# Optimization experiments

Measured on AMD Instinct MI355X. Metric: run time of the kernel, lower is better.

Reference implementation:

```python
import jax, jax.numpy as jnp
import numpy as np

B, H, N, C = 32768, 1024, 4, 1000
BN_EPS = 1e-5        # weighted batch norm epsilon
IG_EPS = 1e-30       # info-gain log epsilon (as in CIGN repo)
TEMPERATURE = 1.0    # routing temperature
BALANCE = 2.0        # information gain balance coefficient


def setup_inputs() -> dict:
    key = jax.random.key(0)
    k = jax.random.split(key, 4)
    return {
        "ig_mask": jax.random.randint(k[0], (B,), 0, 2, dtype=jnp.int32),
        "h_net": jax.random.normal(k[1], (B, H), dtype=jnp.float32),
        "labels": jax.random.randint(k[2], (B,), 0, C, dtype=jnp.int32),
        "gamma": jnp.ones((H,), jnp.float32),
        "beta": jnp.zeros((H,), jnp.float32),
        "W": jax.random.normal(k[3], (H, N), dtype=jnp.float32) * 0.03,
        "b": jnp.zeros((N,), jnp.float32),
    }


def _weighted_batch_norm(x, mask_f, gamma, beta):
    # mask-weighted batch statistics; normalization applied to ALL samples
    w = mask_f[:, None]                       # [B,1]
    wsum = jnp.sum(mask_f)
    mean = jnp.sum(w * x, axis=0) / wsum      # [H]
    var = jnp.sum(w * (x - mean) ** 2, axis=0) / wsum
    return gamma * (x - mean) * jax.lax.rsqrt(var + BN_EPS) + beta


def _info_gain(activations, labels, mask_f):
    sample_count = jnp.sum(mask_f)
    pv = mask_f / sample_count                              # [B]
    p_n_given_x = jax.nn.softmax(activations / TEMPERATURE, axis=1)  # [B,N]
    onehot = jax.nn.one_hot(labels, C, dtype=activations.dtype)      # [B,C]
    # joint p(c,n) = sum_b pv[b] * onehot[b,c] * p_n_given_x[b,n]
    p_cn = jnp.einsum('b,bc,bn->cn', pv, onehot, p_n_given_x)        # [C,N]
    p_n = jnp.sum(p_cn, axis=0)                                      # [N]
    p_c = jnp.sum(p_cn, axis=1)                                      # [C]
    kv = p_cn * (jnp.log(p_cn + IG_EPS)
                 - jnp.log(p_c + IG_EPS)[:, None]
                 - BALANCE * jnp.log(p_n + IG_EPS)[None, :])
    return -jnp.sum(kv)


def reference(ig_mask, h_net, labels, gamma, beta, W, b):
    mask_f = ig_mask.astype(jnp.float32)
    h_normed = _weighted_batch_norm(h_net, mask_f, gamma, beta)      # [B,H]
    activations = h_normed @ W + b                                   # [B,N]
    ig_value = _info_gain(activations, labels, mask_f)               # scalar
    routing = jax.nn.one_hot(jnp.argmax(activations, axis=1), N, dtype=jnp.int32)
    out_routing = jnp.logical_and(routing.astype(bool),
                                  ig_mask[:, None].astype(bool)).astype(jnp.int32)
    return h_normed, ig_value, out_routing
```

## Files before the change

### kernel.cpp

```cpp
#include <hip/hip_runtime.h>
#include <cstddef>

#define B_SZ 32768
#define H_SZ 1024
#define N_SZ 4
#define C_SZ 1000
#define ROW_BLOCKS 2048
#define ROWS_PER_BLOCK 16

#define PART_SUM   0
#define PART_SQ    (PART_SUM + ROW_BLOCKS*H_SZ)
#define WSUM_PART  (PART_SQ  + ROW_BLOCKS*H_SZ)
#define A_OFF      (WSUM_PART + ROW_BLOCKS)
#define C_OFF      (A_OFF + H_SZ)
#define SCAL_OFF   (C_OFF + H_SZ)
#define PCN_OFF    (SCAL_OFF + 8)

#define OUT_IG  ((size_t)B_SZ * H_SZ)
#define OUT_R   (OUT_IG + 1)

__global__ void __launch_bounds__(256) k_colsum(const float* __restrict__ h,
                                                const int* __restrict__ mask,
                                                float* __restrict__ ws) {
    const int rb   = blockIdx.x;
    const int t    = threadIdx.x;
    const int row0 = rb * ROWS_PER_BLOCK;
    const int col  = t * 4;

    if (rb < 500 && t < 8) ws[PCN_OFF + rb * 8 + t] = 0.f;

    float4 sA = make_float4(0.f, 0.f, 0.f, 0.f);
    float4 qA = make_float4(0.f, 0.f, 0.f, 0.f);
    float4 sB = make_float4(0.f, 0.f, 0.f, 0.f);
    float4 qB = make_float4(0.f, 0.f, 0.f, 0.f);
    int mc = 0;

    const float* p = h + (size_t)row0 * H_SZ + col;
#pragma unroll
    for (int r = 0; r < ROWS_PER_BLOCK; r += 2) {
        const int   ma = mask[row0 + r];
        const int   mb = mask[row0 + r + 1];
        const float wa = (float)ma;
        const float wb = (float)mb;
        const float4 xa = *(const float4*)(p);
        const float4 xb = *(const float4*)(p + H_SZ);
        mc += ma + mb;

        float tx;
        tx = wa * xa.x; sA.x += tx; qA.x = fmaf(tx, xa.x, qA.x);
        tx = wa * xa.y; sA.y += tx; qA.y = fmaf(tx, xa.y, qA.y);
        tx = wa * xa.z; sA.z += tx; qA.z = fmaf(tx, xa.z, qA.z);
        tx = wa * xa.w; sA.w += tx; qA.w = fmaf(tx, xa.w, qA.w);

        tx = wb * xb.x; sB.x += tx; qB.x = fmaf(tx, xb.x, qB.x);
        tx = wb * xb.y; sB.y += tx; qB.y = fmaf(tx, xb.y, qB.y);
        tx = wb * xb.z; sB.z += tx; qB.z = fmaf(tx, xb.z, qB.z);
        tx = wb * xb.w; sB.w += tx; qB.w = fmaf(tx, xb.w, qB.w);

        p += 2 * H_SZ;
    }
    sA.x += sB.x; sA.y += sB.y; sA.z += sB.z; sA.w += sB.w;
    qA.x += qB.x; qA.y += qB.y; qA.z += qB.z; qA.w += qB.w;

    *(float4*)(ws + PART_SUM + (size_t)rb * H_SZ + col) = sA;
    *(float4*)(ws + PART_SQ  + (size_t)rb * H_SZ + col) = qA;
    if (t == 0) ws[WSUM_PART + rb] = (float)mc;
}

__global__ void __launch_bounds__(256) k_colfinal(const float* __restrict__ gamma,
                                                  const float* __restrict__ beta,
                                                  float* __restrict__ ws) {
    __shared__ float red[256];
    __shared__ float sh_s[16][17];
    __shared__ float sh_q[16][17];
    const int t = threadIdx.x;

    float w = 0.f;
#pragma unroll
    for (int i = 0; i < ROW_BLOCKS / 256; ++i) w += ws[WSUM_PART + i * 256 + t];
    red[t] = w;
    __syncthreads();
    for (int sft = 128; sft > 0; sft >>= 1) {
        if (t < sft) red[t] += red[t + sft];
        __syncthreads();
    }
    const float wsum = red[0];

    const int c16   = t & 15;
    const int strip = t >> 4;
    const int col   = blockIdx.x * 16 + c16;

    float s = 0.f, q = 0.f;
    const int rb0 = strip * (ROW_BLOCKS / 16);
    for (int k = 0; k < ROW_BLOCKS / 16; ++k) {
        s += ws[PART_SUM + (size_t)(rb0 + k) * H_SZ + col];
        q += ws[PART_SQ  + (size_t)(rb0 + k) * H_SZ + col];
    }
    sh_s[strip][c16] = s;
    sh_q[strip][c16] = q;
    __syncthreads();

    if (t < 16) {
        float S = 0.f, Q = 0.f;
#pragma unroll
        for (int k = 0; k < 16; ++k) { S += sh_s[k][t]; Q += sh_q[k][t]; }
        const int hcol = blockIdx.x * 16 + t;
        const float inv_w = 1.0f / wsum;
        const float mean  = S * inv_w;
        float var = Q * inv_w - mean * mean;
        if (var < 0.f) var = 0.f;
        const float istd = rsqrtf(var + 1e-5f);
        const float a = gamma[hcol] * istd;
        const float c = beta[hcol] - mean * a;
        ws[A_OFF + hcol] = a;
        ws[C_OFF + hcol] = c;
        if (blockIdx.x == 0 && t == 0) ws[SCAL_OFF] = inv_w;
    }
}

__global__ void __launch_bounds__(256, 4) k_fused(const float* __restrict__ hin,
                                                  const int* __restrict__ mask,
                                                  const int* __restrict__ labels,
                                                  const float* __restrict__ W,
                                                  const float* __restrict__ bias,
                                                  const float* __restrict__ ws,
                                                  float* __restrict__ out,
                                                  float* __restrict__ pcn) {
    const int wid  = threadIdx.x >> 6;
    const int lane = threadIdx.x & 63;
    const int gw   = blockIdx.x * 4 + wid;
    const int row0 = gw * 4;

    float4 a4[4], c4[4];
#pragma unroll
    for (int ch = 0; ch < 4; ++ch) {
        const int h = ch * 256 + lane * 4;
        a4[ch] = *(const float4*)(ws + A_OFF + h);
        c4[ch] = *(const float4*)(ws + C_OFF + h);
    }
    const float inv_w = ws[SCAL_OFF];
    const float b0 = bias[0], b1 = bias[1], b2 = bias[2], b3 = bias[3];

    float4 xA[4];
#pragma unroll
    for (int ch = 0; ch < 4; ++ch)
        xA[ch] = *(const float4*)(hin + (size_t)row0 * H_SZ + ch * 256 + lane * 4);

#pragma unroll
    for (int r = 0; r < 4; ++r) {
        const int row = row0 + r;
        float4 xB[4];
        if (r < 3) {
#pragma unroll
            for (int ch = 0; ch < 4; ++ch)
                xB[ch] = *(const float4*)(hin + (size_t)(row + 1) * H_SZ + ch * 256 + lane * 4);
        }

        float acc0 = 0.f, acc1 = 0.f, acc2 = 0.f, acc3 = 0.f;
        float* outr = out + (size_t)row * H_SZ;

#pragma unroll
        for (int ch = 0; ch < 4; ++ch) {
            const int h = ch * 256 + lane * 4;
            float4 hn;
            hn.x = fmaf(xA[ch].x, a4[ch].x, c4[ch].x);
            hn.y = fmaf(xA[ch].y, a4[ch].y, c4[ch].y);
            hn.z = fmaf(xA[ch].z, a4[ch].z, c4[ch].z);
            hn.w = fmaf(xA[ch].w, a4[ch].w, c4[ch].w);
            *(float4*)(outr + h) = hn;

            const float4 w0 = *(const float4*)(W + (size_t)(h + 0) * 4);
            const float4 w1 = *(const float4*)(W + (size_t)(h + 1) * 4);
            const float4 w2 = *(const float4*)(W + (size_t)(h + 2) * 4);
            const float4 w3 = *(const float4*)(W + (size_t)(h + 3) * 4);
            acc0 = fmaf(hn.x, w0.x, acc0); acc1 = fmaf(hn.x, w0.y, acc1);
            acc2 = fmaf(hn.x, w0.z, acc2); acc3 = fmaf(hn.x, w0.w, acc3);
            acc0 = fmaf(hn.y, w1.x, acc0); acc1 = fmaf(hn.y, w1.y, acc1);
            acc2 = fmaf(hn.y, w1.z, acc2); acc3 = fmaf(hn.y, w1.w, acc3);
            acc0 = fmaf(hn.z, w2.x, acc0); acc1 = fmaf(hn.z, w2.y, acc1);
            acc2 = fmaf(hn.z, w2.z, acc2); acc3 = fmaf(hn.z, w2.w, acc3);
            acc0 = fmaf(hn.w, w3.x, acc0); acc1 = fmaf(hn.w, w3.y, acc1);
            acc2 = fmaf(hn.w, w3.z, acc2); acc3 = fmaf(hn.w, w3.w, acc3);
        }

#pragma unroll
        for (int off = 1; off < 64; off <<= 1) {
            acc0 += __shfl_xor(acc0, off);
            acc1 += __shfl_xor(acc1, off);
            acc2 += __shfl_xor(acc2, off);
            acc3 += __shfl_xor(acc3, off);
        }
        acc0 += b0; acc1 += b1; acc2 += b2; acc3 += b3;

        int amax = 0; float best = acc0;
        if (acc1 > best) { best = acc1; amax = 1; }
        if (acc2 > best) { best = acc2; amax = 2; }
        if (acc3 > best) { best = acc3; amax = 3; }

        const float e0 = expf(acc0 - best);
        const float e1 = expf(acc1 - best);
        const float e2 = expf(acc2 - best);
        const float e3 = expf(acc3 - best);
        const float inv = 1.0f / (e0 + e1 + e2 + e3);

        const int m = mask[row];
        if (lane < 4) {
            const float rv = (m && lane == amax) ? 1.0f : 0.0f;
            out[OUT_R + (size_t)row * 4 + lane] = rv;
            if (m) {
                const float pv = (lane == 0 ? e0 : lane == 1 ? e1 : lane == 2 ? e2 : e3)
                                 * inv * inv_w;
                atomicAdd(&pcn[labels[row] * 4 + lane], pv);
            }
        }

        if (r < 3) {
#pragma unroll
            for (int ch = 0; ch < 4; ++ch) xA[ch] = xB[ch];
        }
    }
}

__global__ void __launch_bounds__(256) k_ig(const float* __restrict__ pcn,
                                            float* __restrict__ out) {
    __shared__ float red[256];
    __shared__ float pn_sh[4];
    const int t = threadIdx.x;

    float pn[4] = {0.f, 0.f, 0.f, 0.f};
    for (int c = t; c < C_SZ; c += 256) {
        pn[0] += pcn[c * 4 + 0];
        pn[1] += pcn[c * 4 + 1];
        pn[2] += pcn[c * 4 + 2];
        pn[3] += pcn[c * 4 + 3];
    }
#pragma unroll
    for (int n = 0; n < 4; ++n) {
        red[t] = pn[n];
        __syncthreads();
        for (int sft = 128; sft > 0; sft >>= 1) {
            if (t < sft) red[t] += red[t + sft];
            __syncthreads();
        }
        if (t == 0) pn_sh[n] = red[0];
        __syncthreads();
    }

    const float l0 = 2.0f * logf(pn_sh[0] + 1e-30f);
    const float l1 = 2.0f * logf(pn_sh[1] + 1e-30f);
    const float l2 = 2.0f * logf(pn_sh[2] + 1e-30f);
    const float l3 = 2.0f * logf(pn_sh[3] + 1e-30f);

    float kv = 0.f;
    for (int c = t; c < C_SZ; c += 256) {
        const float v0 = pcn[c * 4 + 0];
        const float v1 = pcn[c * 4 + 1];
        const float v2 = pcn[c * 4 + 2];
        const float v3 = pcn[c * 4 + 3];
        const float pc  = v0 + v1 + v2 + v3;
        const float lpc = logf(pc + 1e-30f);
        kv += v0 * (logf(v0 + 1e-30f) - lpc - l0);
        kv += v1 * (logf(v1 + 1e-30f) - lpc - l1);
        kv += v2 * (logf(v2 + 1e-30f) - lpc - l2);
        kv += v3 * (logf(v3 + 1e-30f) - lpc - l3);
    }
    red[t] = kv;
    __syncthreads();
    for (int sft = 128; sft > 0; sft >>= 1) {
        if (t < sft) red[t] += red[t + sft];
        __syncthreads();
    }
    if (t == 0) out[OUT_IG] = -red[0];
}

extern "C" void kernel_launch(void* const* d_in, const int* in_sizes, int n_in,
                              void* d_out, int out_size, void* d_ws, size_t ws_size,
                              hipStream_t stream) {
    const int*   ig_mask = (const int*)d_in[0];
    const float* h_net   = (const float*)d_in[1];
    const int*   labels  = (const int*)d_in[2];
    const float* gamma   = (const float*)d_in[3];
    const float* beta    = (const float*)d_in[4];
    const float* W       = (const float*)d_in[5];
    const float* b       = (const float*)d_in[6];

    float* out = (float*)d_out;
    float* ws  = (float*)d_ws;

    k_colsum<<<ROW_BLOCKS, 256, 0, stream>>>(h_net, ig_mask, ws);
    k_colfinal<<<H_SZ / 16, 256, 0, stream>>>(gamma, beta, ws);
    k_fused<<<B_SZ / 16, 256, 0, stream>>>(h_net, ig_mask, labels, W, b, ws, out,
                                           ws + PCN_OFF);
    k_ig<<<1, 256, 0, stream>>>(ws + PCN_OFF, out);
}
```

Before: 97.37 us.

## Keep W in registers, batch row reductions, widen colfinal grid

The fused kernel now loads its slice of W into registers once per wave instead of reloading it for every row. It defers the four cross-lane shuffle reductions so they run together after all rows, and it handles the softmax, routing and atomics for 4 rows across 16 lanes instead of serially in 4 lanes. The explicit double-buffered prefetch of the next row is removed and the occupancy hint is lowered from 4 to 3 blocks per SM to allow more registers. Separately, the column-finalize kernel uses 8 columns per block with 32 strips, giving twice as many blocks over the partial-sum reduction.

Measured after the change: 104.7 us. 1.08x slower.

```diff
diff --git a/kernel.cpp b/kernel.cpp
--- a/kernel.cpp
+++ b/kernel.cpp
@@ -71,8 +71,8 @@
                                                   const float* __restrict__ beta,
                                                   float* __restrict__ ws) {
     __shared__ float red[256];
-    __shared__ float sh_s[16][17];
-    __shared__ float sh_q[16][17];
+    __shared__ float sh_s[32][9];
+    __shared__ float sh_q[32][9];
     const int t = threadIdx.x;
 
     float w = 0.f;
@@ -86,25 +86,25 @@
     }
     const float wsum = red[0];
 
-    const int c16   = t & 15;
-    const int strip = t >> 4;
-    const int col   = blockIdx.x * 16 + c16;
+    const int c8    = t & 7;
+    const int strip = t >> 3;
+    const int col   = blockIdx.x * 8 + c8;
 
     float s = 0.f, q = 0.f;
-    const int rb0 = strip * (ROW_BLOCKS / 16);
-    for (int k = 0; k < ROW_BLOCKS / 16; ++k) {
+    const int rb0 = strip * (ROW_BLOCKS / 32);
+    for (int k = 0; k < ROW_BLOCKS / 32; ++k) {
         s += ws[PART_SUM + (size_t)(rb0 + k) * H_SZ + col];
         q += ws[PART_SQ  + (size_t)(rb0 + k) * H_SZ + col];
     }
-    sh_s[strip][c16] = s;
-    sh_q[strip][c16] = q;
+    sh_s[strip][c8] = s;
+    sh_q[strip][c8] = q;
     __syncthreads();
 
-    if (t < 16) {
+    if (t < 8) {
         float S = 0.f, Q = 0.f;
 #pragma unroll
-        for (int k = 0; k < 16; ++k) { S += sh_s[k][t]; Q += sh_q[k][t]; }
-        const int hcol = blockIdx.x * 16 + t;
+        for (int k = 0; k < 32; ++k) { S += sh_s[k][t]; Q += sh_q[k][t]; }
+        const int hcol = blockIdx.x * 8 + t;
         const float inv_w = 1.0f / wsum;
         const float mean  = S * inv_w;
         float var = Q * inv_w - mean * mean;
@@ -118,7 +118,7 @@
     }
 }
 
-__global__ void __launch_bounds__(256, 4) k_fused(const float* __restrict__ hin,
+__global__ void __launch_bounds__(256, 3) k_fused(const float* __restrict__ hin,
                                                   const int* __restrict__ mask,
                                                   const int* __restrict__ labels,
                                                   const float* __restrict__ W,
@@ -131,92 +131,89 @@
     const int gw   = blockIdx.x * 4 + wid;
     const int row0 = gw * 4;
 
+    float4 Wr[4][4];
     float4 a4[4], c4[4];
 #pragma unroll
     for (int ch = 0; ch < 4; ++ch) {
         const int h = ch * 256 + lane * 4;
         a4[ch] = *(const float4*)(ws + A_OFF + h);
         c4[ch] = *(const float4*)(ws + C_OFF + h);
+#pragma unroll
+        for (int j = 0; j < 4; ++j)
+            Wr[ch][j] = *(const float4*)(W + (size_t)(h + j) * 4);
     }
     const float inv_w = ws[SCAL_OFF];
-    const float b0 = bias[0], b1 = bias[1], b2 = bias[2], b3 = bias[3];
-
-    float4 xA[4];
-#pragma unroll
-    for (int ch = 0; ch < 4; ++ch)
-        xA[ch] = *(const float4*)(hin + (size_t)row0 * H_SZ + ch * 256 + lane * 4);
+
+    float4 acc[4];
 
 #pragma unroll
     for (int r = 0; r < 4; ++r) {
         const int row = row0 + r;
-        float4 xB[4];
-        if (r < 3) {
-#pragma unroll
-            for (int ch = 0; ch < 4; ++ch)
-                xB[ch] = *(const float4*)(hin + (size_t)(row + 1) * H_SZ + ch * 256 + lane * 4);
-        }
-
-        float acc0 = 0.f, acc1 = 0.f, acc2 = 0.f, acc3 = 0.f;
-        float* outr = out + (size_t)row * H_SZ;
-
+        const float* xr   = hin + (size_t)row * H_SZ;
+        float*       outr = out + (size_t)row * H_SZ;
+
+        float4 A = make_float4(0.f, 0.f, 0.f, 0.f);
 #pragma unroll
         for (int ch = 0; ch < 4; ++ch) {
             const int h = ch * 256 + lane * 4;
+            const float4 x = *(const float4*)(xr + h);
             float4 hn;
-            hn.x = fmaf(xA[ch].x, a4[ch].x, c4[ch].x);
-            hn.y = fmaf(xA[ch].y, a4[ch].y, c4[ch].y);
-            hn.z = fmaf(xA[ch].z, a4[ch].z, c4[ch].z);
-            hn.w = fmaf(xA[ch].w, a4[ch].w, c4[ch].w);
+            hn.x = fmaf(x.x, a4[ch].x, c4[ch].x);
+            hn.y = fmaf(x.y, a4[ch].y, c4[ch].y);
+            hn.z = fmaf(x.z, a4[ch].z, c4[ch].z);
+            hn.w = fmaf(x.w, a4[ch].w, c4[ch].w);
             *(float4*)(outr + h) = hn;
 
-            const float4 w0 = *(const float4*)(W + (size_t)(h + 0) * 4);
-            const float4 w1 = *(const float4*)(W + (size_t)(h + 1) * 4);
-            const float4 w2 = *(const float4*)(W + (size_t)(h + 2) * 4);
-            const float4 w3 = *(const float4*)(W + (size_t)(h + 3) * 4);
-            acc0 = fmaf(hn.x, w0.x, acc0); acc1 = fmaf(hn.x, w0.y, acc1);
-            acc2 = fmaf(hn.x, w0.z, acc2); acc3 = fmaf(hn.x, w0.w, acc3);
-            acc0 = fmaf(hn.y, w1.x, acc0); acc1 = fmaf(hn.y, w1.y, acc1);
-            acc2 = fmaf(hn.y, w1.z, acc2); acc3 = fmaf(hn.y, w1.w, acc3);
-            acc0 = fmaf(hn.z, w2.x, acc0); acc1 = fmaf(hn.z, w2.y, acc1);
-            acc2 = fmaf(hn.z, w2.z, acc2); acc3 = fmaf(hn.z, w2.w, acc3);
-            acc0 = fmaf(hn.w, w3.x, acc0); acc1 = fmaf(hn.w, w3.y, acc1);
-            acc2 = fmaf(hn.w, w3.z, acc2); acc3 = fmaf(hn.w, w3.w, acc3);
-        }
-
-#pragma unroll
-        for (int off = 1; off < 64; off <<= 1) {
-            acc0 += __shfl_xor(acc0, off);
-            acc1 += __shfl_xor(acc1, off);
-            acc2 += __shfl_xor(acc2, off);
-            acc3 += __shfl_xor(acc3, off);
-        }
-        acc0 += b0; acc1 += b1; acc2 += b2; acc3 += b3;
-
-        int amax = 0; float best = acc0;
-        if (acc1 > best) { best = acc1; amax = 1; }
-        if (acc2 > best) { best = acc2; amax = 2; }
-        if (acc3 > best) { best = acc3; amax = 3; }
-
-        const float e0 = expf(acc0 - best);
-        const float e1 = expf(acc1 - best);
-        const float e2 = expf(acc2 - best);
-        const float e3 = expf(acc3 - best);
+            A.x = fmaf(hn.x, Wr[ch][0].x, A.x); A.y = fmaf(hn.x, Wr[ch][0].y, A.y);
+            A.z = fmaf(hn.x, Wr[ch][0].z, A.z); A.w = fmaf(hn.x, Wr[ch][0].w, A.w);
+            A.x = fmaf(hn.y, Wr[ch][1].x, A.x); A.y = fmaf(hn.y, Wr[ch][1].y, A.y);
+            A.z = fmaf(hn.y, Wr[ch][1].z, A.z); A.w = fmaf(hn.y, Wr[ch][1].w, A.w);
+            A.x = fmaf(hn.z, Wr[ch][2].x, A.x); A.y = fmaf(hn.z, Wr[ch][2].y, A.y);
+            A.z = fmaf(hn.z, Wr[ch][2].z, A.z); A.w = fmaf(hn.z, Wr[ch][2].w, A.w);
+            A.x = fmaf(hn.w, Wr[ch][3].x, A.x); A.y = fmaf(hn.w, Wr[ch][3].y, A.y);
+            A.z = fmaf(hn.w, Wr[ch][3].z, A.z); A.w = fmaf(hn.w, Wr[ch][3].w, A.w);
+        }
+        acc[r] = A;
+    }
+
+#pragma unroll
+    for (int off = 1; off < 64; off <<= 1) {
+#pragma unroll
+        for (int r = 0; r < 4; ++r) {
+            acc[r].x += __shfl_xor(acc[r].x, off);
+            acc[r].y += __shfl_xor(acc[r].y, off);
+            acc[r].z += __shfl_xor(acc[r].z, off);
+            acc[r].w += __shfl_xor(acc[r].w, off);
+        }
+    }
+
+    if (lane < 16) {
+        const int r   = lane >> 2;
+        const int n   = lane & 3;
+        const int row = row0 + r;
+
+        const float s0 = acc[r].x + bias[0];
+        const float s1 = acc[r].y + bias[1];
+        const float s2 = acc[r].z + bias[2];
+        const float s3 = acc[r].w + bias[3];
+
+        int amax = 0; float best = s0;
+        if (s1 > best) { best = s1; amax = 1; }
+        if (s2 > best) { best = s2; amax = 2; }
+        if (s3 > best) { best = s3; amax = 3; }
+
+        const float e0 = expf(s0 - best);
+        const float e1 = expf(s1 - best);
+        const float e2 = expf(s2 - best);
+        const float e3 = expf(s3 - best);
         const float inv = 1.0f / (e0 + e1 + e2 + e3);
 
         const int m = mask[row];
-        if (lane < 4) {
-            const float rv = (m && lane == amax) ? 1.0f : 0.0f;
-            out[OUT_R + (size_t)row * 4 + lane] = rv;
-            if (m) {
-                const float pv = (lane == 0 ? e0 : lane == 1 ? e1 : lane == 2 ? e2 : e3)
-                                 * inv * inv_w;
-                atomicAdd(&pcn[labels[row] * 4 + lane], pv);
-            }
-        }
-
-        if (r < 3) {
-#pragma unroll
-            for (int ch = 0; ch < 4; ++ch) xA[ch] = xB[ch];
+        const float rv = (m && n == amax) ? 1.0f : 0.0f;
+        out[OUT_R + (size_t)row * 4 + n] = rv;
+        if (m) {
+            const float en = (n == 0 ? e0 : n == 1 ? e1 : n == 2 ? e2 : e3);
+            atomicAdd(&pcn[labels[row] * 4 + n], en * inv * inv_w);
         }
     }
 }
@@ -288,7 +285,7 @@
     float* ws  = (float*)d_ws;
 
     k_colsum<<<ROW_BLOCKS, 256, 0, stream>>>(h_net, ig_mask, ws);
-    k_colfinal<<<H_SZ / 16, 256, 0, stream>>>(gamma, beta, ws);
+    k_colfinal<<<H_SZ / 8, 256, 0, stream>>>(gamma, beta, ws);
     k_fused<<<B_SZ / 16, 256, 0, stream>>>(h_net, ig_mask, labels, W, b, ws, out,
                                            ws + PCN_OFF);
     k_ig<<<1, 256, 0, stream>>>(ws + PCN_OFF, out);
```
